# Optimization experiments

Measured on AMD Instinct MI355X. Metric: run time of the kernel, lower is better.

Reference implementation:

```python
import jax, jax.numpy as jnp
import numpy as np

N_NODES = 50000
N_EDGES = 800000
D_IN, D_HID, D_OUT = 64, 64, 1


def gcn_layer(x, src, dst, W, b):
    """GCN conv: linear transform, then degree-normalized scatter-add over edges
    (with self-loops), matching x' = D^-1/2 (A+I) D^-1/2 X W^T + b."""
    n = x.shape[0]
    h = x @ W.T + b                                   # [N, out]
    deg = jax.ops.segment_sum(jnp.ones_like(dst, dtype=h.dtype), dst,
                              num_segments=n) + 1.0   # +1 for self-loop
    inv_sqrt_deg = jax.lax.rsqrt(deg)                 # [N]
    coef = inv_sqrt_deg[src] * inv_sqrt_deg[dst]      # [E]
    msgs = h[src] * coef[:, None]                     # gather + scale
    agg = jax.ops.segment_sum(msgs, dst, num_segments=n)   # scatter-add
    agg = agg + h * (inv_sqrt_deg * inv_sqrt_deg)[:, None]  # self-loop term
    return agg


def setup_inputs() -> dict:
    key = jax.random.key(0)
    k = jax.random.split(key, 9)
    x = jax.random.normal(k[0], (N_NODES, D_IN), dtype=jnp.float32)
    edge_index = jax.random.randint(k[1], (2, N_EDGES), 0, N_NODES, dtype=jnp.int64)
    s = 0.1
    W0 = jax.random.normal(k[2], (D_HID, D_IN), dtype=jnp.float32) * s
    b0 = jnp.zeros((D_HID,), dtype=jnp.float32)
    W1 = jax.random.normal(k[3], (D_HID, D_HID), dtype=jnp.float32) * s
    b1 = jnp.zeros((D_HID,), dtype=jnp.float32)
    W2 = jax.random.normal(k[4], (D_OUT, D_HID), dtype=jnp.float32) * s
    b2 = jnp.zeros((D_OUT,), dtype=jnp.float32)
    return {"x": x, "edge_index": edge_index,
            "W0": W0, "b0": b0, "W1": W1, "b1": b1, "W2": W2, "b2": b2}


def reference(x, edge_index, W0, b0, W1, b1, W2, b2):
    src, dst = edge_index[0], edge_index[1]
    h = jax.nn.relu(gcn_layer(x, src, dst, W0, b0))
    h = jax.nn.relu(gcn_layer(h, src, dst, W1, b1))
    out = gcn_layer(h, src, dst, W2, b2)   # [N, 1] per-node logits
    return out
```

## Files before the change

### kernel.cpp

```cpp
#include <hip/hip_runtime.h>

#define N_NODES 50000
#define N_EDGES 800000
#define DMAX 64
#define ZROW N_NODES
#define NB 196
#define CELL 40
#define P1_BLKS 512
#define LIN_BLKS 3125
typedef unsigned short u16;

__global__ __launch_bounds__(256) void bin_lin0_k(
    const int* __restrict__ src, const int* __restrict__ dst,
    unsigned* __restrict__ payload, unsigned char* __restrict__ counts,
    const float* __restrict__ x, const float* __restrict__ W,
    const float* __restrict__ b, float* __restrict__ h)
{
    __shared__ float4 smem4[2009];
    int bid = blockIdx.x;
    int tid = threadIdx.x;
    if (bid < P1_BLKS) {
        unsigned* cur = (unsigned*)smem4;
        unsigned* pay = cur + NB;
        for (int i = tid; i < NB; i += 256) cur[i] = 0;
        __syncthreads();
        const int4* dst4 = (const int4*)dst;
        const int4* src4 = (const int4*)src;
        const int NQ = N_EDGES / 4;
        for (int q = bid * 256 + tid; q < NQ; q += P1_BLKS * 256) {
            int4 d = dst4[q];
            int4 s = src4[q];
#define BIN(dd, ss)                                                        \
            {                                                              \
                int bkt = (dd) >> 8;                                       \
                unsigned v = ((unsigned)(ss) << 8) | ((unsigned)(dd) & 255u); \
                int p = atomicAdd((int*)&cur[bkt], 1);                     \
                if (p < CELL) pay[bkt * CELL + p] = v;                     \
            }
            BIN(d.x, s.x) BIN(d.y, s.y) BIN(d.z, s.z) BIN(d.w, s.w)
#undef BIN
        }
        __syncthreads();
        unsigned* pg = payload + (size_t)bid * (NB * CELL);
        for (int i = tid; i < NB * CELL; i += 256) pg[i] = pay[i];
        for (int i = tid; i < NB; i += 256)
            counts[bid * NB + i] = (unsigned char)min((int)cur[i], CELL);
    } else {
        float* Ws = (float*)smem4;
        float* xs = (float*)smem4 + 64 * 68;
        int j = tid & 63, ln = tid >> 6;
        int nb = (bid - P1_BLKS) * 16;
        const float4* W4 = (const float4*)W;
#pragma unroll
        for (int i = 0; i < 4; ++i) {
            int idx4 = i * 256 + tid;
            *(float4*)&Ws[(idx4 >> 4) * 68 + (idx4 & 15) * 4] = W4[idx4];
        }
        {
            const float4* x4 = (const float4*)(x + (size_t)nb * 64);
            float4 v = x4[tid];
            *(float4*)&xs[(tid >> 4) * 68 + (tid & 15) * 4] = v;
        }
        __syncthreads();
        float a0 = b[j], a1 = a0, a2 = a0, a3 = a0;
        const float4* wp = (const float4*)&Ws[j * 68];
        const float4* p0 = (const float4*)&xs[(ln * 4 + 0) * 68];
        const float4* p1 = (const float4*)&xs[(ln * 4 + 1) * 68];
        const float4* p2 = (const float4*)&xs[(ln * 4 + 2) * 68];
        const float4* p3 = (const float4*)&xs[(ln * 4 + 3) * 68];
#pragma unroll
        for (int k4 = 0; k4 < 16; ++k4) {
            float4 w = wp[k4];
            float4 q0 = p0[k4]; a0 += w.x*q0.x + w.y*q0.y + w.z*q0.z + w.w*q0.w;
            float4 q1 = p1[k4]; a1 += w.x*q1.x + w.y*q1.y + w.z*q1.z + w.w*q1.w;
            float4 q2 = p2[k4]; a2 += w.x*q2.x + w.y*q2.y + w.z*q2.z + w.w*q2.w;
            float4 q3 = p3[k4]; a3 += w.x*q3.x + w.y*q3.y + w.z*q3.z + w.w*q3.w;
        }
        h[(size_t)(nb + ln * 4 + 0) * 64 + j] = a0;
        h[(size_t)(nb + ln * 4 + 1) * 64 + j] = a1;
        h[(size_t)(nb + ln * 4 + 2) * 64 + j] = a2;
        h[(size_t)(nb + ln * 4 + 3) * 64 + j] = a3;
    }
}

__global__ __launch_bounds__(256) void place_k(
    const unsigned* __restrict__ payload, const unsigned char* __restrict__ counts,
    int* __restrict__ cnt, u16* __restrict__ csr)
{
    __shared__ int cur[256];
    int b = blockIdx.x, tid = threadIdx.x;
    cur[tid] = 0;
    __syncthreads();
    int base = b << 8;
    for (int sb = tid; sb < P1_BLKS; sb += 256) {
        int c = counts[sb * NB + b];
        const unsigned* cell = payload + ((size_t)sb * NB + b) * CELL;
        for (int k = 0; k < c; ++k) {
            unsigned v = cell[k];
            int loc = (int)(v & 255u);
            int s = (int)(v >> 8);
            int slot = atomicAdd(&cur[loc], 1);
            if (slot < DMAX) csr[(size_t)(base + loc) * 64 + slot] = (u16)s;
        }
    }
    __syncthreads();
    int n = base + tid;
    if (n < N_NODES) cnt[n] = cur[tid];
}

__global__ __launch_bounds__(256) void prep_k(const int* __restrict__ cnt,
                                              u16* __restrict__ csr,
                                              float* __restrict__ bufA,
                                              float* __restrict__ bufB) {
    int tid = threadIdx.x, j = tid & 63, w = tid >> 6;
    int n = blockIdx.x * 4 + w;
    if (blockIdx.x == 0 && tid < 64) {
        bufA[(size_t)ZROW * 64 + tid] = 0.f;
        bufB[(size_t)ZROW * 64 + tid] = 0.f;
    }
    if (n >= N_NODES) return;
    int mf = cnt[n];
    float invn = rsqrtf((float)mf + 1.f);
    bufA[(size_t)n * 64 + j] *= invn;
    int m = min(mf, DMAX);
    int mp = min((m + 15) & ~15, DMAX);
    if (j >= m && j < mp) csr[(size_t)n * 64 + j] = (u16)ZROW;
}

#define GATHER64(hbuf, n, m16, sum_out)                                     \
    int s_l = (int)csr[(size_t)(n) * 64 + j];                               \
    float acc0 = hbuf[(size_t)(n) * 64 + j];                                \
    float acc1 = 0.f, acc2 = 0.f, acc3 = 0.f;                               \
    _Pragma("unroll 1")                                                     \
    for (int i = 0; i < (m16); i += 16) {                                   \
        int s0 = __builtin_amdgcn_readlane(s_l, i);                         \
        int s1 = __builtin_amdgcn_readlane(s_l, i + 1);                     \
        int s2 = __builtin_amdgcn_readlane(s_l, i + 2);                     \
        int s3 = __builtin_amdgcn_readlane(s_l, i + 3);                     \
        int s4 = __builtin_amdgcn_readlane(s_l, i + 4);                     \
        int s5 = __builtin_amdgcn_readlane(s_l, i + 5);                     \
        int s6 = __builtin_amdgcn_readlane(s_l, i + 6);                     \
        int s7 = __builtin_amdgcn_readlane(s_l, i + 7);                     \
        int s8 = __builtin_amdgcn_readlane(s_l, i + 8);                     \
        int s9 = __builtin_amdgcn_readlane(s_l, i + 9);                     \
        int sA = __builtin_amdgcn_readlane(s_l, i + 10);                    \
        int sB = __builtin_amdgcn_readlane(s_l, i + 11);                    \
        int sC = __builtin_amdgcn_readlane(s_l, i + 12);                    \
        int sD = __builtin_amdgcn_readlane(s_l, i + 13);                    \
        int sE = __builtin_amdgcn_readlane(s_l, i + 14);                    \
        int sF = __builtin_amdgcn_readlane(s_l, i + 15);                    \
        float v0 = hbuf[((size_t)s0 << 6) + j];                             \
        float v1 = hbuf[((size_t)s1 << 6) + j];                             \
        float v2 = hbuf[((size_t)s2 << 6) + j];                             \
        float v3 = hbuf[((size_t)s3 << 6) + j];                             \
        float v4 = hbuf[((size_t)s4 << 6) + j];                             \
        float v5 = hbuf[((size_t)s5 << 6) + j];                             \
        float v6 = hbuf[((size_t)s6 << 6) + j];                             \
        float v7 = hbuf[((size_t)s7 << 6) + j];                             \
        float v8 = hbuf[((size_t)s8 << 6) + j];                             \
        float v9 = hbuf[((size_t)s9 << 6) + j];                             \
        float vA = hbuf[((size_t)sA << 6) + j];                             \
        float vB = hbuf[((size_t)sB << 6) + j];                             \
        float vC = hbuf[((size_t)sC << 6) + j];                             \
        float vD = hbuf[((size_t)sD << 6) + j];                             \
        float vE = hbuf[((size_t)sE << 6) + j];                             \
        float vF = hbuf[((size_t)sF << 6) + j];                             \
        acc0 += v0; acc1 += v1; acc2 += v2; acc3 += v3;                     \
        acc0 += v4; acc1 += v5; acc2 += v6; acc3 += v7;                     \
        acc0 += v8; acc1 += v9; acc2 += vA; acc3 += vB;                     \
        acc0 += vC; acc1 += vD; acc2 += vE; acc3 += vF;                     \
    }                                                                       \
    float sum_out = (acc0 + acc1) + (acc2 + acc3);

__global__ __launch_bounds__(256) void gl_k(const float* __restrict__ h,
                                            const int* __restrict__ cnt,
                                            const u16* __restrict__ csr,
                                            const float* __restrict__ W,
                                            const float* __restrict__ b,
                                            float* __restrict__ out) {
    __shared__ float Ws[64 * 68];
    __shared__ float rs[4][68];
    int tid = threadIdx.x, j = tid & 63, w = tid >> 6;
    int nb = blockIdx.x * 16;
    const float4* W4 = (const float4*)W;
#pragma unroll
    for (int i = 0; i < 4; ++i) {
        int idx4 = i * 256 + tid;
        *(float4*)&Ws[(idx4 >> 4) * 68 + (idx4 & 15) * 4] = W4[idx4];
    }
    __syncthreads();
    const float4* wp = (const float4*)&Ws[j * 68];
    float bj = b[j];
#pragma unroll 1
    for (int t = 0; t < 4; ++t) {
        int n = nb + w * 4 + t;
        int mf = cnt[n];
        float invn = rsqrtf((float)mf + 1.f);
        int m16 = min((min(mf, DMAX) + 15) & ~15, DMAX);
        GATHER64(h, n, m16, sum)
        rs[w][j] = fmaxf(sum * invn, 0.f);
        __builtin_amdgcn_wave_barrier();
        float o0 = bj, o1 = 0.f;
        const float4* rp = (const float4*)&rs[w][0];
#pragma unroll
        for (int k4 = 0; k4 < 16; k4 += 2) {
            float4 w0 = wp[k4],     q0 = rp[k4];
            float4 w1 = wp[k4 + 1], q1 = rp[k4 + 1];
            o0 += w0.x*q0.x + w0.y*q0.y + w0.z*q0.z + w0.w*q0.w;
            o1 += w1.x*q1.x + w1.y*q1.y + w1.z*q1.z + w1.w*q1.w;
        }
        __builtin_amdgcn_wave_barrier();
        out[(size_t)n * 64 + j] = (o0 + o1) * invn;
    }
}

__global__ __launch_bounds__(256) void gd_k(const float* __restrict__ h,
                                            const int* __restrict__ cnt,
                                            const u16* __restrict__ csr,
                                            const float* __restrict__ W2,
                                            const float* __restrict__ b2,
                                            float* __restrict__ h2) {
    int tid = threadIdx.x, j = tid & 63, w = tid >> 6;
    int nb = blockIdx.x * 16;
    float w2 = W2[j], b2s = b2[0];
#pragma unroll 1
    for (int t = 0; t < 4; ++t) {
        int n = nb + w * 4 + t;
        int mf = cnt[n];
        float invn = rsqrtf((float)mf + 1.f);
        int m16 = min((min(mf, DMAX) + 15) & ~15, DMAX);
        GATHER64(h, n, m16, sum)
        float pp = fmaxf(sum * invn, 0.f) * w2;
#pragma unroll
        for (int off = 32; off; off >>= 1) pp += __shfl_xor(pp, off, 64);
        if (j == 0) h2[n] = (pp + b2s) * invn;
    }
}

__global__ __launch_bounds__(256) void g1_k(const float* __restrict__ h2,
                                            const int* __restrict__ cnt,
                                            const u16* __restrict__ csr,
                                            float* __restrict__ out) {
    int tid = threadIdx.x, j = tid & 63, w = tid >> 6;
    int nb = blockIdx.x * 16;
#pragma unroll 1
    for (int t = 0; t < 4; ++t) {
        int n = nb + w * 4 + t;
        int mf = cnt[n];
        int m = min(mf, DMAX);
        float invn = rsqrtf((float)mf + 1.f);
        float v = 0.f;
        if (j < m) v = h2[(int)csr[(size_t)n * 64 + j]];
#pragma unroll
        for (int off = 32; off; off >>= 1) v += __shfl_xor(v, off, 64);
        if (j == 0) out[n] = (v + h2[n]) * invn;
    }
}

extern "C" void kernel_launch(void* const* d_in, const int* in_sizes, int n_in,
                              void* d_out, int out_size, void* d_ws, size_t ws_size,
                              hipStream_t stream) {
    const float* x  = (const float*)d_in[0];
    const int*   ei = (const int*)d_in[1];
    const float* W0 = (const float*)d_in[2];
    const float* b0 = (const float*)d_in[3];
    const float* W1 = (const float*)d_in[4];
    const float* b1 = (const float*)d_in[5];
    const float* W2 = (const float*)d_in[6];
    const float* b2 = (const float*)d_in[7];
    float* out = (float*)d_out;

    char* ws = (char*)d_ws;
    size_t off = 0;
    auto alloc = [&](size_t bytes) {
        void* p = ws + off;
        off = (off + bytes + 255) & ~(size_t)255;
        return p;
    };
    int*      cnt     = (int*)alloc((size_t)N_NODES * 4);
    u16*      csr     = (u16*)alloc((size_t)N_NODES * DMAX * 2);
    float*    bufA    = (float*)alloc((size_t)(N_NODES + 1) * 64 * 4);
    float*    bufB    = (float*)alloc((size_t)(N_NODES + 1) * 64 * 4);
    float*    h2      = (float*)alloc((size_t)N_NODES * 4);
    unsigned* payload = (unsigned*)alloc((size_t)P1_BLKS * NB * CELL * 4);
    unsigned char* counts = (unsigned char*)alloc((size_t)P1_BLKS * NB);

    const int* src = ei;
    const int* dst = ei + N_EDGES;

    bin_lin0_k<<<P1_BLKS + LIN_BLKS, 256, 0, stream>>>(src, dst, payload, counts,
                                                       x, W0, b0, bufA);
    place_k<<<NB, 256, 0, stream>>>(payload, counts, cnt, csr);
    prep_k<<<(N_NODES + 3) / 4, 256, 0, stream>>>(cnt, csr, bufA, bufB);
    gl_k<<<LIN_BLKS, 256, 0, stream>>>(bufA, cnt, csr, W1, b1, bufB);
    gd_k<<<LIN_BLKS, 256, 0, stream>>>(bufB, cnt, csr, W2, b2, h2);
    g1_k<<<LIN_BLKS, 256, 0, stream>>>(h2, cnt, csr, out);
}
```

Before: 109.9 us.

## Store hidden features in bf16 and fold prep pass into place kernel

Hidden activations are now stored as bf16, which halves the bytes moved by the edge gathers. The gather loop is rewritten so each lane loads a packed pair of features for one of two neighbors, and the two half-waves are combined with a shuffle. The separate prep kernel, which scaled rows by the inverse degree, padded the CSR and zeroed the sentinel row, is merged into place_k, removing one launch and one pass over the features. In exchange, bf16 rounding of intermediate activations lowers accuracy, and the scaling now runs in only 196 blocks.

```diff
diff --git a/kernel.cpp b/kernel.cpp
--- a/kernel.cpp
+++ b/kernel.cpp
@@ -10,11 +10,23 @@
 #define LIN_BLKS 3125
 typedef unsigned short u16;
 
+__device__ __forceinline__ u16 f2bf(float f) {
+    unsigned u = __builtin_bit_cast(unsigned, f);
+    u += 0x7FFFu + ((u >> 16) & 1u);
+    return (u16)(u >> 16);
+}
+__device__ __forceinline__ float bflo(unsigned u) {
+    return __builtin_bit_cast(float, u << 16);
+}
+__device__ __forceinline__ float bfhi(unsigned u) {
+    return __builtin_bit_cast(float, u & 0xFFFF0000u);
+}
+
 __global__ __launch_bounds__(256) void bin_lin0_k(
     const int* __restrict__ src, const int* __restrict__ dst,
     unsigned* __restrict__ payload, unsigned char* __restrict__ counts,
     const float* __restrict__ x, const float* __restrict__ W,
-    const float* __restrict__ b, float* __restrict__ h)
+    const float* __restrict__ b, u16* __restrict__ hA)
 {
     __shared__ float4 smem4[2009];
     int bid = blockIdx.x;
@@ -76,16 +88,17 @@
             float4 q2 = p2[k4]; a2 += w.x*q2.x + w.y*q2.y + w.z*q2.z + w.w*q2.w;
             float4 q3 = p3[k4]; a3 += w.x*q3.x + w.y*q3.y + w.z*q3.z + w.w*q3.w;
         }
-        h[(size_t)(nb + ln * 4 + 0) * 64 + j] = a0;
-        h[(size_t)(nb + ln * 4 + 1) * 64 + j] = a1;
-        h[(size_t)(nb + ln * 4 + 2) * 64 + j] = a2;
-        h[(size_t)(nb + ln * 4 + 3) * 64 + j] = a3;
+        hA[(size_t)(nb + ln * 4 + 0) * 64 + j] = f2bf(a0);
+        hA[(size_t)(nb + ln * 4 + 1) * 64 + j] = f2bf(a1);
+        hA[(size_t)(nb + ln * 4 + 2) * 64 + j] = f2bf(a2);
+        hA[(size_t)(nb + ln * 4 + 3) * 64 + j] = f2bf(a3);
     }
 }
 
 __global__ __launch_bounds__(256) void place_k(
     const unsigned* __restrict__ payload, const unsigned char* __restrict__ counts,
-    int* __restrict__ cnt, u16* __restrict__ csr)
+    int* __restrict__ cnt, u16* __restrict__ csr,
+    u16* __restrict__ hA, u16* __restrict__ hB)
 {
     __shared__ int cur[256];
     int b = blockIdx.x, tid = threadIdx.x;
@@ -98,89 +111,77 @@
         for (int k = 0; k < c; ++k) {
             unsigned v = cell[k];
             int loc = (int)(v & 255u);
-            int s = (int)(v >> 8);
             int slot = atomicAdd(&cur[loc], 1);
-            if (slot < DMAX) csr[(size_t)(base + loc) * 64 + slot] = (u16)s;
+            if (slot < DMAX) csr[(size_t)(base + loc) * 64 + slot] = (u16)(v >> 8);
         }
     }
     __syncthreads();
     int n = base + tid;
-    if (n < N_NODES) cnt[n] = cur[tid];
-}
-
-__global__ __launch_bounds__(256) void prep_k(const int* __restrict__ cnt,
-                                              u16* __restrict__ csr,
-                                              float* __restrict__ bufA,
-                                              float* __restrict__ bufB) {
-    int tid = threadIdx.x, j = tid & 63, w = tid >> 6;
-    int n = blockIdx.x * 4 + w;
-    if (blockIdx.x == 0 && tid < 64) {
-        bufA[(size_t)ZROW * 64 + tid] = 0.f;
-        bufB[(size_t)ZROW * 64 + tid] = 0.f;
-    }
-    if (n >= N_NODES) return;
-    int mf = cnt[n];
-    float invn = rsqrtf((float)mf + 1.f);
-    bufA[(size_t)n * 64 + j] *= invn;
-    int m = min(mf, DMAX);
-    int mp = min((m + 15) & ~15, DMAX);
-    if (j >= m && j < mp) csr[(size_t)n * 64 + j] = (u16)ZROW;
-}
-
-#define GATHER64(hbuf, n, m16, sum_out)                                     \
+    if (n < N_NODES) {
+        int c = cur[tid];
+        cnt[n] = c;
+        int m = min(c, DMAX);
+        int mp = min((m + 15) & ~15, DMAX);
+        for (int k = m; k < mp; ++k) csr[(size_t)n * 64 + k] = (u16)ZROW;
+    }
+    unsigned* hA32 = (unsigned*)hA;
+    int col = tid & 31, r0 = tid >> 5;
+    for (int it = 0; it < 32; ++it) {
+        int rl = r0 + (it << 3);
+        int n2 = base + rl;
+        if (n2 < N_NODES) {
+            float invn = rsqrtf((float)cur[rl] + 1.f);
+            unsigned u = hA32[(size_t)n2 * 32 + col];
+            float lo = bflo(u) * invn;
+            float hi = bfhi(u) * invn;
+            hA32[(size_t)n2 * 32 + col] = ((unsigned)f2bf(hi) << 16) | f2bf(lo);
+        }
+    }
+    if (b == 0 && tid < 32) {
+        ((unsigned*)hA)[(size_t)ZROW * 32 + tid] = 0;
+        ((unsigned*)hB)[(size_t)ZROW * 32 + tid] = 0;
+    }
+}
+
+#define PAIRB(k, AX, AY)                                                    \
+    {                                                                       \
+        int sa = __builtin_amdgcn_readlane(s_l, i + 2*(k));                 \
+        int sb = __builtin_amdgcn_readlane(s_l, i + 2*(k) + 1);             \
+        int ss = hsel ? sb : sa;                                            \
+        unsigned uu = *(const unsigned*)(hb + (((size_t)ss) << 6) + fp);    \
+        AX += bflo(uu); AY += bfhi(uu);                                     \
+    }
+
+#define GATHERB(hb, n, m16, TX, TY)                                         \
     int s_l = (int)csr[(size_t)(n) * 64 + j];                               \
-    float acc0 = hbuf[(size_t)(n) * 64 + j];                                \
-    float acc1 = 0.f, acc2 = 0.f, acc3 = 0.f;                               \
+    float ax0=0.f, ay0=0.f, ax1=0.f, ay1=0.f;                               \
+    float ax2=0.f, ay2=0.f, ax3=0.f, ay3=0.f;                               \
     _Pragma("unroll 1")                                                     \
     for (int i = 0; i < (m16); i += 16) {                                   \
-        int s0 = __builtin_amdgcn_readlane(s_l, i);                         \
-        int s1 = __builtin_amdgcn_readlane(s_l, i + 1);                     \
-        int s2 = __builtin_amdgcn_readlane(s_l, i + 2);                     \
-        int s3 = __builtin_amdgcn_readlane(s_l, i + 3);                     \
-        int s4 = __builtin_amdgcn_readlane(s_l, i + 4);                     \
-        int s5 = __builtin_amdgcn_readlane(s_l, i + 5);                     \
-        int s6 = __builtin_amdgcn_readlane(s_l, i + 6);                     \
-        int s7 = __builtin_amdgcn_readlane(s_l, i + 7);                     \
-        int s8 = __builtin_amdgcn_readlane(s_l, i + 8);                     \
-        int s9 = __builtin_amdgcn_readlane(s_l, i + 9);                     \
-        int sA = __builtin_amdgcn_readlane(s_l, i + 10);                    \
-        int sB = __builtin_amdgcn_readlane(s_l, i + 11);                    \
-        int sC = __builtin_amdgcn_readlane(s_l, i + 12);                    \
-        int sD = __builtin_amdgcn_readlane(s_l, i + 13);                    \
-        int sE = __builtin_amdgcn_readlane(s_l, i + 14);                    \
-        int sF = __builtin_amdgcn_readlane(s_l, i + 15);                    \
-        float v0 = hbuf[((size_t)s0 << 6) + j];                             \
-        float v1 = hbuf[((size_t)s1 << 6) + j];                             \
-        float v2 = hbuf[((size_t)s2 << 6) + j];                             \
-        float v3 = hbuf[((size_t)s3 << 6) + j];                             \
-        float v4 = hbuf[((size_t)s4 << 6) + j];                             \
-        float v5 = hbuf[((size_t)s5 << 6) + j];                             \
-        float v6 = hbuf[((size_t)s6 << 6) + j];                             \
-        float v7 = hbuf[((size_t)s7 << 6) + j];                             \
-        float v8 = hbuf[((size_t)s8 << 6) + j];                             \
-        float v9 = hbuf[((size_t)s9 << 6) + j];                             \
-        float vA = hbuf[((size_t)sA << 6) + j];                             \
-        float vB = hbuf[((size_t)sB << 6) + j];                             \
-        float vC = hbuf[((size_t)sC << 6) + j];                             \
-        float vD = hbuf[((size_t)sD << 6) + j];                             \
-        float vE = hbuf[((size_t)sE << 6) + j];                             \
-        float vF = hbuf[((size_t)sF << 6) + j];                             \
-        acc0 += v0; acc1 += v1; acc2 += v2; acc3 += v3;                     \
-        acc0 += v4; acc1 += v5; acc2 += v6; acc3 += v7;                     \
-        acc0 += v8; acc1 += v9; acc2 += vA; acc3 += vB;                     \
-        acc0 += vC; acc1 += vD; acc2 += vE; acc3 += vF;                     \
+        PAIRB(0, ax0, ay0) PAIRB(1, ax1, ay1)                               \
+        PAIRB(2, ax2, ay2) PAIRB(3, ax3, ay3)                               \
+        PAIRB(4, ax0, ay0) PAIRB(5, ax1, ay1)                               \
+        PAIRB(6, ax2, ay2) PAIRB(7, ax3, ay3)                               \
     }                                                                       \
-    float sum_out = (acc0 + acc1) + (acc2 + acc3);
-
-__global__ __launch_bounds__(256) void gl_k(const float* __restrict__ h,
+    float TX = (ax0 + ax1) + (ax2 + ax3);                                   \
+    float TY = (ay0 + ay1) + (ay2 + ay3);                                   \
+    TX += __shfl_xor(TX, 32, 64);                                           \
+    TY += __shfl_xor(TY, 32, 64);                                           \
+    {                                                                       \
+        unsigned su = *(const unsigned*)(hb + (((size_t)(n)) << 6) + fp);   \
+        TX += bflo(su); TY += bfhi(su);                                     \
+    }
+
+__global__ __launch_bounds__(256) void gl_k(const u16* __restrict__ hb,
                                             const int* __restrict__ cnt,
                                             const u16* __restrict__ csr,
                                             const float* __restrict__ W,
                                             const float* __restrict__ b,
-                                            float* __restrict__ out) {
+                                            u16* __restrict__ outb) {
     __shared__ float Ws[64 * 68];
     __shared__ float rs[4][68];
     int tid = threadIdx.x, j = tid & 63, w = tid >> 6;
+    int fp = (j & 31) * 2, hsel = j >> 5;
     int nb = blockIdx.x * 16;
     const float4* W4 = (const float4*)W;
 #pragma unroll
@@ -197,8 +198,11 @@
         int mf = cnt[n];
         float invn = rsqrtf((float)mf + 1.f);
         int m16 = min((min(mf, DMAX) + 15) & ~15, DMAX);
-        GATHER64(h, n, m16, sum)
-        rs[w][j] = fmaxf(sum * invn, 0.f);
+        GATHERB(hb, n, m16, tx, ty)
+        if (j < 32) {
+            rs[w][fp]     = fmaxf(tx * invn, 0.f);
+            rs[w][fp + 1] = fmaxf(ty * invn, 0.f);
+        }
         __builtin_amdgcn_wave_barrier();
         float o0 = bj, o1 = 0.f;
         const float4* rp = (const float4*)&rs[w][0];
@@ -210,30 +214,31 @@
             o1 += w1.x*q1.x + w1.y*q1.y + w1.z*q1.z + w1.w*q1.w;
         }
         __builtin_amdgcn_wave_barrier();
-        out[(size_t)n * 64 + j] = (o0 + o1) * invn;
-    }
-}
-
-__global__ __launch_bounds__(256) void gd_k(const float* __restrict__ h,
+        outb[(size_t)n * 64 + j] = f2bf((o0 + o1) * invn);
+    }
+}
+
+__global__ __launch_bounds__(256) void gd_k(const u16* __restrict__ hb,
                                             const int* __restrict__ cnt,
                                             const u16* __restrict__ csr,
                                             const float* __restrict__ W2,
                                             const float* __restrict__ b2,
                                             float* __restrict__ h2) {
     int tid = threadIdx.x, j = tid & 63, w = tid >> 6;
+    int fp = (j & 31) * 2, hsel = j >> 5;
     int nb = blockIdx.x * 16;
-    float w2 = W2[j], b2s = b2[0];
+    float w2x = W2[fp], w2y = W2[fp + 1], b2s = b2[0];
 #pragma unroll 1
     for (int t = 0; t < 4; ++t) {
         int n = nb + w * 4 + t;
         int mf = cnt[n];
         float invn = rsqrtf((float)mf + 1.f);
         int m16 = min((min(mf, DMAX) + 15) & ~15, DMAX);
-        GATHER64(h, n, m16, sum)
-        float pp = fmaxf(sum * invn, 0.f) * w2;
-#pragma unroll
-        for (int off = 32; off; off >>= 1) pp += __shfl_xor(pp, off, 64);
-        if (j == 0) h2[n] = (pp + b2s) * invn;
+        GATHERB(hb, n, m16, tx, ty)
+        float c = fmaxf(tx * invn, 0.f) * w2x + fmaxf(ty * invn, 0.f) * w2y;
+#pragma unroll
+        for (int off = 16; off; off >>= 1) c += __shfl_xor(c, off, 64);
+        if (j == 0) h2[n] = (c + b2s) * invn;
     }
 }
 
@@ -277,11 +282,11 @@
         off = (off + bytes + 255) & ~(size_t)255;
         return p;
     };
-    int*      cnt     = (int*)alloc((size_t)N_NODES * 4);
-    u16*      csr     = (u16*)alloc((size_t)N_NODES * DMAX * 2);
-    float*    bufA    = (float*)alloc((size_t)(N_NODES + 1) * 64 * 4);
-    float*    bufB    = (float*)alloc((size_t)(N_NODES + 1) * 64 * 4);
-    float*    h2      = (float*)alloc((size_t)N_NODES * 4);
+    int*      cnt  = (int*)alloc((size_t)N_NODES * 4);
+    u16*      csr  = (u16*)alloc((size_t)N_NODES * DMAX * 2);
+    u16*      hA   = (u16*)alloc((size_t)(N_NODES + 1) * 64 * 2);
+    u16*      hB   = (u16*)alloc((size_t)(N_NODES + 1) * 64 * 2);
+    float*    h2   = (float*)alloc((size_t)N_NODES * 4);
     unsigned* payload = (unsigned*)alloc((size_t)P1_BLKS * NB * CELL * 4);
     unsigned char* counts = (unsigned char*)alloc((size_t)P1_BLKS * NB);
 
@@ -289,10 +294,9 @@
     const int* dst = ei + N_EDGES;
 
     bin_lin0_k<<<P1_BLKS + LIN_BLKS, 256, 0, stream>>>(src, dst, payload, counts,
-                                                       x, W0, b0, bufA);
-    place_k<<<NB, 256, 0, stream>>>(payload, counts, cnt, csr);
-    prep_k<<<(N_NODES + 3) / 4, 256, 0, stream>>>(cnt, csr, bufA, bufB);
-    gl_k<<<LIN_BLKS, 256, 0, stream>>>(bufA, cnt, csr, W1, b1, bufB);
-    gd_k<<<LIN_BLKS, 256, 0, stream>>>(bufB, cnt, csr, W2, b2, h2);
+                                                       x, W0, b0, hA);
+    place_k<<<NB, 256, 0, stream>>>(payload, counts, cnt, csr, hA, hB);
+    gl_k<<<LIN_BLKS, 256, 0, stream>>>(hA, cnt, csr, W1, b1, hB);
+    gd_k<<<LIN_BLKS, 256, 0, stream>>>(hB, cnt, csr, W2, b2, h2);
     g1_k<<<LIN_BLKS, 256, 0, stream>>>(h2, cnt, csr, out);
 }
```

New measurement: 109.3 us. About the same (-0.5%).
